# Kernel tuning notes

Hardware: AMD Instinct MI355X
Metric: run time of the kernel (lower is better)

The kernel has to match this reference:

```python
import jax, jax.numpy as jnp
import numpy as np


def setup_inputs() -> dict:
    key = jax.random.key(0)
    k_x, k_in, k_rec, k_out = jax.random.split(key, 4)
    B, T, H, C = 1024, 784, 512, 10
    inputs = jax.random.normal(k_x, (B, T), dtype=jnp.float32)
    # kaiming_normal_ for relu on a (H, 1) weight: std = sqrt(2 / fan_in) = sqrt(2)
    W_in = jax.random.normal(k_in, (H, 1), dtype=jnp.float32) * jnp.sqrt(2.0)
    # henaff_init_ makes an orthogonal recurrent kernel; emulate with a random
    # orthogonal matrix (same math class: orthogonal recurrence)
    A = jax.random.normal(k_rec, (H, H), dtype=jnp.float32)
    Q, _ = jnp.linalg.qr(A)
    W_rec = Q.astype(jnp.float32)
    W_out = jax.random.normal(k_out, (C, H), dtype=jnp.float32) * (1.0 / jnp.sqrt(H))
    b_out = jnp.zeros((C,), dtype=jnp.float32)
    # exact permutation the torch module builds: RandomState(92916).permutation(784)
    permutation = jnp.asarray(np.random.RandomState(92916).permutation(T), dtype=jnp.int32)
    return {"inputs": inputs, "W_in": W_in, "W_rec": W_rec,
            "W_out": W_out, "b_out": b_out, "permutation": permutation}


def reference(inputs, W_in, W_rec, W_out, b_out, permutation):
    # inputs: [B, T]; the module always permutes (self.permute is truthy)
    x = inputs[:, permutation]                    # [B, T]
    xs = x.T                                      # [T, B], scan over time
    w_in = W_in[:, 0]                             # [H]
    B = inputs.shape[0]
    H = W_rec.shape[0]
    h0 = jnp.zeros((B, H), dtype=inputs.dtype)

    def step(h, x_t):
        # input_kernel(x_t[:,None]) = outer(x_t, w_in); recurrent = h @ W_rec.T
        h_new = jax.nn.relu(x_t[:, None] * w_in[None, :] + h @ W_rec.T)
        return h_new, None

    h_last, _ = jax.lax.scan(step, h0, xs)
    return h_last @ W_out.T + b_out               # [B, 10]
```

## Files before the change

kernel.cpp:

```cpp
#include <hip/hip_runtime.h>

typedef _Float16 f16;
typedef __attribute__((ext_vector_type(8))) _Float16 f16x8;
typedef __attribute__((ext_vector_type(4))) _Float16 f16x4;
typedef __attribute__((ext_vector_type(4))) float f32x4;

#define T_STEPS 784
#define HDIM    512
#define COUT    10

#define XH_OFF   (512 * 1024)
#define WS_NEED  ((size_t)(XH_OFF + T_STEPS * 1024 * 2))

#define MFMA16(a, b, c) __builtin_amdgcn_mfma_f32_16x16x32_f16((a), (b), (c), 0, 0, 0)
#define BAR_LGKM() asm volatile("s_waitcnt lgkmcnt(0)\n\ts_barrier" ::: "memory")

__global__ void cvt_w(const float* __restrict__ W, f16* __restrict__ Wf) {
    const int c  = blockIdx.x * 256 + threadIdx.x;
    const int l  = c & 63;
    const int kk = (c >> 6) & 15;
    const int n  = (c >> 10) & 3;
    const int w  = c >> 12;
    const int row = w * 64 + n * 16 + (l & 15);
    const int col = kk * 32 + (l >> 4) * 8;
    const float* s = W + row * HDIM + col;
    f16* d = Wf + (size_t)c * 8;
#pragma unroll
    for (int j = 0; j < 8; ++j) d[j] = (f16)s[j];
}

__global__ void permute_x(const float* __restrict__ x, const int* __restrict__ perm,
                          f16* __restrict__ xh) {
    const int i = blockIdx.x * 256 + threadIdx.x;
    const int t = i >> 10, b = i & 1023;
    xh[i] = (f16)x[b * T_STEPS + perm[t]];
}

__global__ __launch_bounds__(512, 2)
void rnn_l2(const float* __restrict__ W_in, const f16* __restrict__ Wf,
            const f16* __restrict__ xh, const float* __restrict__ W_out,
            const float* __restrict__ b_out, float* __restrict__ out)
{
    __shared__ __align__(16) char lds[147456];
    char* const HB = lds + 131072;

    const int tid  = threadIdx.x;
    const int w    = tid >> 6;
    const int lane = tid & 63;
    const int b_   = lane & 15;
    const int lhi  = lane >> 4;
    const int b0   = blockIdx.x * 16;

    const f16* wb = Wf + (size_t)w * 32768 + lane * 8;
#define LDW(kk, n) (*(const f16x8*)(wb + ((n) * 16 + (kk)) * 512))

#pragma unroll
    for (int n = 0; n < 4; ++n)
#pragma unroll
        for (int ck = 0; ck < 4; ++ck)
            *(f16x8*)(lds + (((w * 4 + n) * 4 + ck) * 1024) + lane * 16) = LDW(ck, n);

    for (int i = tid; i < 4096; i += 512) ((int*)HB)[i] = 0;

    f16x4 win[4];
#pragma unroll
    for (int n = 0; n < 4; ++n)
#pragma unroll
        for (int r = 0; r < 4; ++r)
            win[n][r] = (f16)W_in[w * 64 + n * 16 + lhi * 4 + r];

    char* const rb = HB + lane * 16;
    int wa[4];
#pragma unroll
    for (int n = 0; n < 4; ++n)
        wa[n] = (2 * w + (n >> 1)) * 1024
              + (((((n & 1) * 2 + (lhi >> 1)) << 4) | b_) * 16)
              + (lhi & 1) * 8;

    const int rot = (int)((blockIdx.x * 7u) % 12u);
    int ks[12];
#pragma unroll
    for (int i = 0; i < 12; ++i) {
        int v = i + rot; if (v >= 12) v -= 12;
        ks[i] = 4 + v;
    }

    __syncthreads();

    f16x8 r0[4], r1[4], r2[4], r3[4];
#pragma unroll
    for (int n = 0; n < 4; ++n) r0[n] = LDW(ks[0], n);
#pragma unroll
    for (int n = 0; n < 4; ++n) r1[n] = LDW(ks[1], n);
#pragma unroll
    for (int n = 0; n < 4; ++n) r2[n] = LDW(ks[2], n);
#pragma unroll
    for (int n = 0; n < 4; ++n) r3[n] = LDW(ks[3], n);

#define STEP_KK(kki, RING, nxtk)                                    \
    {                                                               \
        const f16x8 bh = *(const f16x8*)(rb + (kki) * 1024);        \
        acc0 = MFMA16(RING[0], bh, acc0);                           \
        acc1 = MFMA16(RING[1], bh, acc1);                           \
        acc2 = MFMA16(RING[2], bh, acc2);                           \
        acc3 = MFMA16(RING[3], bh, acc3);                           \
        RING[0] = LDW(nxtk, 0); RING[1] = LDW(nxtk, 1);             \
        RING[2] = LDW(nxtk, 2); RING[3] = LDW(nxtk, 3);             \
    }
#define CACHED_KK(ck)                                               \
    {                                                               \
        const f16x8 bh = *(const f16x8*)(rb + (ck) * 1024);         \
        const f16x8 a0 = *(const f16x8*)(lds + (((w * 4 + 0) * 4 + (ck)) * 1024) + lane * 16); \
        const f16x8 a1 = *(const f16x8*)(lds + (((w * 4 + 1) * 4 + (ck)) * 1024) + lane * 16); \
        const f16x8 a2 = *(const f16x8*)(lds + (((w * 4 + 2) * 4 + (ck)) * 1024) + lane * 16); \
        const f16x8 a3 = *(const f16x8*)(lds + (((w * 4 + 3) * 4 + (ck)) * 1024) + lane * 16); \
        acc0 = MFMA16(a0, bh, acc0);                                \
        acc1 = MFMA16(a1, bh, acc1);                                \
        acc2 = MFMA16(a2, bh, acc2);                                \
        acc3 = MFMA16(a3, bh, acc3);                                \
    }

#pragma unroll 1
    for (int t = 0; t < T_STEPS; ++t) {
        const float xv = (float)xh[t * 1024 + b0 + b_];

        f32x4 acc0 = {0.f, 0.f, 0.f, 0.f};
        f32x4 acc1 = {0.f, 0.f, 0.f, 0.f};
        f32x4 acc2 = {0.f, 0.f, 0.f, 0.f};
        f32x4 acc3 = {0.f, 0.f, 0.f, 0.f};

        CACHED_KK(0) CACHED_KK(1) CACHED_KK(2) CACHED_KK(3)
        STEP_KK(ks[0], r0, ks[4])   STEP_KK(ks[1], r1, ks[5])
        STEP_KK(ks[2], r2, ks[6])   STEP_KK(ks[3], r3, ks[7])
        STEP_KK(ks[4], r0, ks[8])   STEP_KK(ks[5], r1, ks[9])
        STEP_KK(ks[6], r2, ks[10])  STEP_KK(ks[7], r3, ks[11])
        STEP_KK(ks[8], r0, ks[0])   STEP_KK(ks[9], r1, ks[1])
        STEP_KK(ks[10], r2, ks[2])  STEP_KK(ks[11], r3, ks[3])

        BAR_LGKM();

        {
            f16x4 hv;
            float v;
#define EPI(n, ACC)                                                  \
            v = ACC[0] + xv * (float)win[n][0]; hv[0] = (f16)fmaxf(v, 0.f); \
            v = ACC[1] + xv * (float)win[n][1]; hv[1] = (f16)fmaxf(v, 0.f); \
            v = ACC[2] + xv * (float)win[n][2]; hv[2] = (f16)fmaxf(v, 0.f); \
            v = ACC[3] + xv * (float)win[n][3]; hv[3] = (f16)fmaxf(v, 0.f); \
            *(f16x4*)(HB + wa[n]) = hv;
            EPI(0, acc0) EPI(1, acc1) EPI(2, acc2) EPI(3, acc3)
#undef EPI
        }

        BAR_LGKM();
    }

    if (tid < 16 * COUT) {
        const int bb = tid / COUT, c = tid % COUT;
        float s_ = b_out[c];
        const float* wo = W_out + c * HDIM;
#pragma unroll 4
        for (int o0 = 0; o0 < HDIM; o0 += 8) {
            const int off = (o0 >> 5) * 1024 + (((((o0 >> 3) & 3) << 4) | bb) * 16);
            f16x8 hv = *(const f16x8*)(HB + off);
#pragma unroll
            for (int jj = 0; jj < 8; ++jj)
                s_ += (float)hv[jj] * wo[o0 + jj];
        }
        out[(b0 + bb) * COUT + c] = s_;
    }
}

extern "C" void kernel_launch(void* const* d_in, const int* in_sizes, int n_in,
                              void* d_out, int out_size, void* d_ws, size_t ws_size,
                              hipStream_t stream)
{
    (void)in_sizes; (void)n_in; (void)out_size; (void)ws_size;
    const float* x     = (const float*)d_in[0];
    const float* W_in  = (const float*)d_in[1];
    const float* W_rec = (const float*)d_in[2];
    const float* W_out = (const float*)d_in[3];
    const float* b_out = (const float*)d_in[4];
    const int*   perm  = (const int*)d_in[5];
    float* out = (float*)d_out;

    f16* Wf  = (f16*)d_ws;
    f16* xhp = (f16*)((char*)d_ws + XH_OFF);

    cvt_w<<<dim3(128), dim3(256), 0, stream>>>(W_rec, Wf);
    permute_x<<<dim3(T_STEPS * 1024 / 256), dim3(256), 0, stream>>>(x, perm, xhp);
    rnn_l2<<<dim3(64), dim3(512), 0, stream>>>(W_in, Wf, xhp, W_out, b_out, out);
}
```

Baseline: 1.206 ms.

## Keep first four K-slices of W_rec in registers and double-buffer hidden state

Moves the first four K-chunks of the recurrent weight from LDS into 16 persistent VGPR vectors, so those MFMAs no longer issue LDS reads. Also double-buffers the hidden-state tile in LDS, which removes one of the two barriers per timestep. The cost is much higher register pressure at launch_bounds(512,2), which could cause spills or fewer waves per SIMD, plus a larger hidden-state buffer.

```diff
diff --git a/kernel.cpp b/kernel.cpp
--- a/kernel.cpp
+++ b/kernel.cpp
@@ -10,7 +10,6 @@
 #define COUT    10
 
 #define XH_OFF   (512 * 1024)
-#define WS_NEED  ((size_t)(XH_OFF + T_STEPS * 1024 * 2))
 
 #define MFMA16(a, b, c) __builtin_amdgcn_mfma_f32_16x16x32_f16((a), (b), (c), 0, 0, 0)
 #define BAR_LGKM() asm volatile("s_waitcnt lgkmcnt(0)\n\ts_barrier" ::: "memory")
@@ -37,13 +36,11 @@
 }
 
 __global__ __launch_bounds__(512, 2)
-void rnn_l2(const float* __restrict__ W_in, const f16* __restrict__ Wf,
-            const f16* __restrict__ xh, const float* __restrict__ W_out,
-            const float* __restrict__ b_out, float* __restrict__ out)
+void rnn_res(const float* __restrict__ W_in, const f16* __restrict__ Wf,
+             const f16* __restrict__ xh, const float* __restrict__ W_out,
+             const float* __restrict__ b_out, float* __restrict__ out)
 {
-    __shared__ __align__(16) char lds[147456];
-    char* const HB = lds + 131072;
-
+    __shared__ __align__(16) char hb[32768];
     const int tid  = threadIdx.x;
     const int w    = tid >> 6;
     const int lane = tid & 63;
@@ -51,16 +48,19 @@
     const int lhi  = lane >> 4;
     const int b0   = blockIdx.x * 16;
 
+    for (int i = tid; i < 4096; i += 512) ((int*)hb)[i] = 0;
+
     const f16* wb = Wf + (size_t)w * 32768 + lane * 8;
 #define LDW(kk, n) (*(const f16x8*)(wb + ((n) * 16 + (kk)) * 512))
 
+    f16x8 wr[16];
 #pragma unroll
-    for (int n = 0; n < 4; ++n)
+    for (int kk = 0; kk < 4; ++kk)
 #pragma unroll
-        for (int ck = 0; ck < 4; ++ck)
-            *(f16x8*)(lds + (((w * 4 + n) * 4 + ck) * 1024) + lane * 16) = LDW(ck, n);
-
-    for (int i = tid; i < 4096; i += 512) ((int*)HB)[i] = 0;
+        for (int n = 0; n < 4; ++n)
+            wr[kk * 4 + n] = LDW(kk, n);
+#pragma unroll
+    for (int i = 0; i < 16; ++i) asm volatile("" : "+v"(wr[i]));
 
     f16x4 win[4];
 #pragma unroll
@@ -69,7 +69,7 @@
         for (int r = 0; r < 4; ++r)
             win[n][r] = (f16)W_in[w * 64 + n * 16 + lhi * 4 + r];
 
-    char* const rb = HB + lane * 16;
+    char* const rb = hb + lane * 16;
     int wa[4];
 #pragma unroll
     for (int n = 0; n < 4; ++n)
@@ -97,9 +97,17 @@
 #pragma unroll
     for (int n = 0; n < 4; ++n) r3[n] = LDW(ks[3], n);
 
+#define RES_KK(ck)                                                  \
+    {                                                               \
+        const f16x8 bh = *(const f16x8*)(rp + (ck) * 1024);         \
+        acc0 = MFMA16(wr[(ck) * 4 + 0], bh, acc0);                  \
+        acc1 = MFMA16(wr[(ck) * 4 + 1], bh, acc1);                  \
+        acc2 = MFMA16(wr[(ck) * 4 + 2], bh, acc2);                  \
+        acc3 = MFMA16(wr[(ck) * 4 + 3], bh, acc3);                  \
+    }
 #define STEP_KK(kki, RING, nxtk)                                    \
     {                                                               \
-        const f16x8 bh = *(const f16x8*)(rb + (kki) * 1024);        \
+        const f16x8 bh = *(const f16x8*)(rp + (kki) * 1024);        \
         acc0 = MFMA16(RING[0], bh, acc0);                           \
         acc1 = MFMA16(RING[1], bh, acc1);                           \
         acc2 = MFMA16(RING[2], bh, acc2);                           \
@@ -107,37 +115,26 @@
         RING[0] = LDW(nxtk, 0); RING[1] = LDW(nxtk, 1);             \
         RING[2] = LDW(nxtk, 2); RING[3] = LDW(nxtk, 3);             \
     }
-#define CACHED_KK(ck)                                               \
-    {                                                               \
-        const f16x8 bh = *(const f16x8*)(rb + (ck) * 1024);         \
-        const f16x8 a0 = *(const f16x8*)(lds + (((w * 4 + 0) * 4 + (ck)) * 1024) + lane * 16); \
-        const f16x8 a1 = *(const f16x8*)(lds + (((w * 4 + 1) * 4 + (ck)) * 1024) + lane * 16); \
-        const f16x8 a2 = *(const f16x8*)(lds + (((w * 4 + 2) * 4 + (ck)) * 1024) + lane * 16); \
-        const f16x8 a3 = *(const f16x8*)(lds + (((w * 4 + 3) * 4 + (ck)) * 1024) + lane * 16); \
-        acc0 = MFMA16(a0, bh, acc0);                                \
-        acc1 = MFMA16(a1, bh, acc1);                                \
-        acc2 = MFMA16(a2, bh, acc2);                                \
-        acc3 = MFMA16(a3, bh, acc3);                                \
-    }
 
+    int cur = 0;
 #pragma unroll 1
     for (int t = 0; t < T_STEPS; ++t) {
         const float xv = (float)xh[t * 1024 + b0 + b_];
+        const char* rp = rb + cur;
+        char* wq = hb + (cur ^ 16384);
 
         f32x4 acc0 = {0.f, 0.f, 0.f, 0.f};
         f32x4 acc1 = {0.f, 0.f, 0.f, 0.f};
         f32x4 acc2 = {0.f, 0.f, 0.f, 0.f};
         f32x4 acc3 = {0.f, 0.f, 0.f, 0.f};
 
-        CACHED_KK(0) CACHED_KK(1) CACHED_KK(2) CACHED_KK(3)
+        RES_KK(0) RES_KK(1) RES_KK(2) RES_KK(3)
         STEP_KK(ks[0], r0, ks[4])   STEP_KK(ks[1], r1, ks[5])
         STEP_KK(ks[2], r2, ks[6])   STEP_KK(ks[3], r3, ks[7])
         STEP_KK(ks[4], r0, ks[8])   STEP_KK(ks[5], r1, ks[9])
         STEP_KK(ks[6], r2, ks[10])  STEP_KK(ks[7], r3, ks[11])
         STEP_KK(ks[8], r0, ks[0])   STEP_KK(ks[9], r1, ks[1])
         STEP_KK(ks[10], r2, ks[2])  STEP_KK(ks[11], r3, ks[3])
-
-        BAR_LGKM();
 
         {
             f16x4 hv;
@@ -147,22 +144,24 @@
             v = ACC[1] + xv * (float)win[n][1]; hv[1] = (f16)fmaxf(v, 0.f); \
             v = ACC[2] + xv * (float)win[n][2]; hv[2] = (f16)fmaxf(v, 0.f); \
             v = ACC[3] + xv * (float)win[n][3]; hv[3] = (f16)fmaxf(v, 0.f); \
-            *(f16x4*)(HB + wa[n]) = hv;
+            *(f16x4*)(wq + wa[n]) = hv;
             EPI(0, acc0) EPI(1, acc1) EPI(2, acc2) EPI(3, acc3)
 #undef EPI
         }
 
         BAR_LGKM();
+        cur ^= 16384;
     }
 
     if (tid < 16 * COUT) {
         const int bb = tid / COUT, c = tid % COUT;
+        const char* hr = hb + cur;
         float s_ = b_out[c];
         const float* wo = W_out + c * HDIM;
 #pragma unroll 4
         for (int o0 = 0; o0 < HDIM; o0 += 8) {
             const int off = (o0 >> 5) * 1024 + (((((o0 >> 3) & 3) << 4) | bb) * 16);
-            f16x8 hv = *(const f16x8*)(HB + off);
+            f16x8 hv = *(const f16x8*)(hr + off);
 #pragma unroll
             for (int jj = 0; jj < 8; ++jj)
                 s_ += (float)hv[jj] * wo[o0 + jj];
@@ -189,5 +188,5 @@
 
     cvt_w<<<dim3(128), dim3(256), 0, stream>>>(W_rec, Wf);
     permute_x<<<dim3(T_STEPS * 1024 / 256), dim3(256), 0, stream>>>(x, perm, xhp);
-    rnn_l2<<<dim3(64), dim3(512), 0, stream>>>(W_in, Wf, xhp, W_out, b_out, out);
+    rnn_res<<<dim3(64), dim3(512), 0, stream>>>(W_in, Wf, xhp, W_out, b_out, out);
 }
```

Result: slower. 2.859 ms (+137.2%).

## Process two 16-row batch tiles per block to reuse streamed W_rec fragments

Applied to the files above, without the earlier changes.

Each block now handles 32 batch rows instead of 16, splitting them into two 16-row MFMA tiles that share the same W_rec A-fragments from registers, LDS and global memory. The grid is halved to 32 blocks, so the per-step global stream of W_rec is amortised over twice the batch work. In exchange, each wave runs twice as many MFMAs per step on the serial recurrence, and only 32 of the many CUs stay busy. The LDS hidden-state buffer doubles, which likely drops occupancy to one block per CU.

```diff
diff --git a/kernel.cpp b/kernel.cpp
--- a/kernel.cpp
+++ b/kernel.cpp
@@ -10,7 +10,6 @@
 #define COUT    10
 
 #define XH_OFF   (512 * 1024)
-#define WS_NEED  ((size_t)(XH_OFF + T_STEPS * 1024 * 2))
 
 #define MFMA16(a, b, c) __builtin_amdgcn_mfma_f32_16x16x32_f16((a), (b), (c), 0, 0, 0)
 #define BAR_LGKM() asm volatile("s_waitcnt lgkmcnt(0)\n\ts_barrier" ::: "memory")
@@ -41,7 +40,7 @@
             const f16* __restrict__ xh, const float* __restrict__ W_out,
             const float* __restrict__ b_out, float* __restrict__ out)
 {
-    __shared__ __align__(16) char lds[147456];
+    __shared__ __align__(16) char lds[163840];
     char* const HB = lds + 131072;
 
     const int tid  = threadIdx.x;
@@ -49,7 +48,7 @@
     const int lane = tid & 63;
     const int b_   = lane & 15;
     const int lhi  = lane >> 4;
-    const int b0   = blockIdx.x * 16;
+    const int b0   = blockIdx.x * 32;
 
     const f16* wb = Wf + (size_t)w * 32768 + lane * 8;
 #define LDW(kk, n) (*(const f16x8*)(wb + ((n) * 16 + (kk)) * 512))
@@ -60,7 +59,7 @@
         for (int ck = 0; ck < 4; ++ck)
             *(f16x8*)(lds + (((w * 4 + n) * 4 + ck) * 1024) + lane * 16) = LDW(ck, n);
 
-    for (int i = tid; i < 4096; i += 512) ((int*)HB)[i] = 0;
+    for (int i = tid; i < 8192; i += 512) ((int*)HB)[i] = 0;
 
     f16x4 win[4];
 #pragma unroll
@@ -99,35 +98,47 @@
 
 #define STEP_KK(kki, RING, nxtk)                                    \
     {                                                               \
-        const f16x8 bh = *(const f16x8*)(rb + (kki) * 1024);        \
-        acc0 = MFMA16(RING[0], bh, acc0);                           \
-        acc1 = MFMA16(RING[1], bh, acc1);                           \
-        acc2 = MFMA16(RING[2], bh, acc2);                           \
-        acc3 = MFMA16(RING[3], bh, acc3);                           \
+        const f16x8 bhA = *(const f16x8*)(rp + (kki) * 1024);       \
+        const f16x8 bhB = *(const f16x8*)(rp + 16384 + (kki) * 1024); \
+        aA0 = MFMA16(RING[0], bhA, aA0);                            \
+        aA1 = MFMA16(RING[1], bhA, aA1);                            \
+        aA2 = MFMA16(RING[2], bhA, aA2);                            \
+        aA3 = MFMA16(RING[3], bhA, aA3);                            \
+        aB0 = MFMA16(RING[0], bhB, aB0);                            \
+        aB1 = MFMA16(RING[1], bhB, aB1);                            \
+        aB2 = MFMA16(RING[2], bhB, aB2);                            \
+        aB3 = MFMA16(RING[3], bhB, aB3);                            \
         RING[0] = LDW(nxtk, 0); RING[1] = LDW(nxtk, 1);             \
         RING[2] = LDW(nxtk, 2); RING[3] = LDW(nxtk, 3);             \
     }
 #define CACHED_KK(ck)                                               \
     {                                                               \
-        const f16x8 bh = *(const f16x8*)(rb + (ck) * 1024);         \
+        const f16x8 bhA = *(const f16x8*)(rp + (ck) * 1024);        \
+        const f16x8 bhB = *(const f16x8*)(rp + 16384 + (ck) * 1024);\
         const f16x8 a0 = *(const f16x8*)(lds + (((w * 4 + 0) * 4 + (ck)) * 1024) + lane * 16); \
         const f16x8 a1 = *(const f16x8*)(lds + (((w * 4 + 1) * 4 + (ck)) * 1024) + lane * 16); \
         const f16x8 a2 = *(const f16x8*)(lds + (((w * 4 + 2) * 4 + (ck)) * 1024) + lane * 16); \
         const f16x8 a3 = *(const f16x8*)(lds + (((w * 4 + 3) * 4 + (ck)) * 1024) + lane * 16); \
-        acc0 = MFMA16(a0, bh, acc0);                                \
-        acc1 = MFMA16(a1, bh, acc1);                                \
-        acc2 = MFMA16(a2, bh, acc2);                                \
-        acc3 = MFMA16(a3, bh, acc3);                                \
+        aA0 = MFMA16(a0, bhA, aA0);                                 \
+        aA1 = MFMA16(a1, bhA, aA1);                                 \
+        aA2 = MFMA16(a2, bhA, aA2);                                 \
+        aA3 = MFMA16(a3, bhA, aA3);                                 \
+        aB0 = MFMA16(a0, bhB, aB0);                                 \
+        aB1 = MFMA16(a1, bhB, aB1);                                 \
+        aB2 = MFMA16(a2, bhB, aB2);                                 \
+        aB3 = MFMA16(a3, bhB, aB3);                                 \
     }
 
 #pragma unroll 1
     for (int t = 0; t < T_STEPS; ++t) {
-        const float xv = (float)xh[t * 1024 + b0 + b_];
-
-        f32x4 acc0 = {0.f, 0.f, 0.f, 0.f};
-        f32x4 acc1 = {0.f, 0.f, 0.f, 0.f};
-        f32x4 acc2 = {0.f, 0.f, 0.f, 0.f};
-        f32x4 acc3 = {0.f, 0.f, 0.f, 0.f};
+        const float xvA = (float)xh[t * 1024 + b0 + b_];
+        const float xvB = (float)xh[t * 1024 + b0 + 16 + b_];
+        const char* rp = rb;
+
+        f32x4 aA0 = {0.f, 0.f, 0.f, 0.f}, aA1 = {0.f, 0.f, 0.f, 0.f};
+        f32x4 aA2 = {0.f, 0.f, 0.f, 0.f}, aA3 = {0.f, 0.f, 0.f, 0.f};
+        f32x4 aB0 = {0.f, 0.f, 0.f, 0.f}, aB1 = {0.f, 0.f, 0.f, 0.f};
+        f32x4 aB2 = {0.f, 0.f, 0.f, 0.f}, aB3 = {0.f, 0.f, 0.f, 0.f};
 
         CACHED_KK(0) CACHED_KK(1) CACHED_KK(2) CACHED_KK(3)
         STEP_KK(ks[0], r0, ks[4])   STEP_KK(ks[1], r1, ks[5])
@@ -142,27 +153,34 @@
         {
             f16x4 hv;
             float v;
-#define EPI(n, ACC)                                                  \
-            v = ACC[0] + xv * (float)win[n][0]; hv[0] = (f16)fmaxf(v, 0.f); \
-            v = ACC[1] + xv * (float)win[n][1]; hv[1] = (f16)fmaxf(v, 0.f); \
-            v = ACC[2] + xv * (float)win[n][2]; hv[2] = (f16)fmaxf(v, 0.f); \
-            v = ACC[3] + xv * (float)win[n][3]; hv[3] = (f16)fmaxf(v, 0.f); \
-            *(f16x4*)(HB + wa[n]) = hv;
-            EPI(0, acc0) EPI(1, acc1) EPI(2, acc2) EPI(3, acc3)
-#undef EPI
+#define EPI2(n, ACCA, ACCB)                                          \
+            v = ACCA[0] + xvA * (float)win[n][0]; hv[0] = (f16)fmaxf(v, 0.f); \
+            v = ACCA[1] + xvA * (float)win[n][1]; hv[1] = (f16)fmaxf(v, 0.f); \
+            v = ACCA[2] + xvA * (float)win[n][2]; hv[2] = (f16)fmaxf(v, 0.f); \
+            v = ACCA[3] + xvA * (float)win[n][3]; hv[3] = (f16)fmaxf(v, 0.f); \
+            *(f16x4*)(HB + wa[n]) = hv;                              \
+            v = ACCB[0] + xvB * (float)win[n][0]; hv[0] = (f16)fmaxf(v, 0.f); \
+            v = ACCB[1] + xvB * (float)win[n][1]; hv[1] = (f16)fmaxf(v, 0.f); \
+            v = ACCB[2] + xvB * (float)win[n][2]; hv[2] = (f16)fmaxf(v, 0.f); \
+            v = ACCB[3] + xvB * (float)win[n][3]; hv[3] = (f16)fmaxf(v, 0.f); \
+            *(f16x4*)(HB + 16384 + wa[n]) = hv;
+            EPI2(0, aA0, aB0) EPI2(1, aA1, aB1) EPI2(2, aA2, aB2) EPI2(3, aA3, aB3)
+#undef EPI2
         }
 
         BAR_LGKM();
     }
 
-    if (tid < 16 * COUT) {
+    if (tid < 32 * COUT) {
         const int bb = tid / COUT, c = tid % COUT;
+        const char* hr = HB + (bb >> 4) * 16384;
+        const int bl = bb & 15;
         float s_ = b_out[c];
         const float* wo = W_out + c * HDIM;
 #pragma unroll 4
         for (int o0 = 0; o0 < HDIM; o0 += 8) {
-            const int off = (o0 >> 5) * 1024 + (((((o0 >> 3) & 3) << 4) | bb) * 16);
-            f16x8 hv = *(const f16x8*)(HB + off);
+            const int off = (o0 >> 5) * 1024 + (((((o0 >> 3) & 3) << 4) | bl) * 16);
+            f16x8 hv = *(const f16x8*)(hr + off);
 #pragma unroll
             for (int jj = 0; jj < 8; ++jj)
                 s_ += (float)hv[jj] * wo[o0 + jj];
@@ -189,5 +207,5 @@
 
     cvt_w<<<dim3(128), dim3(256), 0, stream>>>(W_rec, Wf);
     permute_x<<<dim3(T_STEPS * 1024 / 256), dim3(256), 0, stream>>>(x, perm, xhp);
-    rnn_l2<<<dim3(64), dim3(512), 0, stream>>>(W_in, Wf, xhp, W_out, b_out, out);
-}
+    rnn_l2<<<dim3(32), dim3(512), 0, stream>>>(W_in, Wf, xhp, W_out, b_out, out);
+}
```

After: 2.678 ms. +122.1%, slower.
